# Performance work log

Hardware: AMD Instinct MI355X
Metric: run time of the kernel (lower is better)

## Reference

```python
import jax, jax.numpy as jnp
import numpy as np

B, T, H = 32, 2048, 1024

def setup_inputs() -> dict:
    key = jax.random.key(0)
    k1, k2, k3 = jax.random.split(key, 3)
    gru_output = jax.random.normal(k1, (B, T, H), dtype=jnp.float32)
    # Xavier uniform bounds
    lim_w = float(np.sqrt(6.0 / (H + H)))
    lim_c = float(np.sqrt(6.0 / (H + 1)))
    attention_weights = jax.random.uniform(k2, (H, H), minval=-lim_w, maxval=lim_w, dtype=jnp.float32)
    context_vector = jax.random.uniform(k3, (H, 1), minval=-lim_c, maxval=lim_c, dtype=jnp.float32)
    return {"gru_output": gru_output, "attention_weights": attention_weights, "context_vector": context_vector}

def reference(gru_output, attention_weights, context_vector):
    # score: [B, T, H]
    score = jnp.tanh(jnp.einsum('bth,hk->btk', gru_output, attention_weights))
    # logits: [B, T]
    logits = jnp.einsum('bth,h->bt', score, context_vector[:, 0])
    attn = jax.nn.softmax(logits, axis=1)  # over time dim
    # context: [B, H]
    context = jnp.einsum('bth,bt->bh', gru_output, attn)
    return (context, attn)
```

## Files before the change

kernel.cpp:

```cpp
#include <hip/hip_runtime.h>
#include <hip/hip_bf16.h>
#include <stdint.h>

#define B_DIM 32
#define T_DIM 2048
#define H_DIM 1024
#define M_DIM (B_DIM * T_DIM)
#define K_DIM H_DIM
#define N_DIM H_DIM
#define BK 32

typedef __attribute__((ext_vector_type(4))) float f32x4;
typedef __attribute__((ext_vector_type(8))) short short8;

__device__ __forceinline__ unsigned short f2bf(float x) {
  unsigned u = __float_as_uint(x);
  unsigned r = (u + 0x7FFFu + ((u >> 16) & 1u)) >> 16;
  return (unsigned short)r;
}

__device__ __forceinline__ float fast_tanh(float x) {
  x = fminf(fmaxf(x, -15.f), 15.f);
  float e = __expf(2.f * x);
  return (e - 1.f) / (e + 1.f);
}

__global__ void convert_g_kernel(const float* __restrict__ in,
                                 unsigned short* __restrict__ out) {
  size_t base = ((size_t)blockIdx.x * 256 + threadIdx.x) * 8;
  const float4* p = (const float4*)(in + base);
  float4 u0 = p[0];
  float4 u1 = p[1];
  short8 s;
  s[0] = (short)f2bf(u0.x); s[1] = (short)f2bf(u0.y);
  s[2] = (short)f2bf(u0.z); s[3] = (short)f2bf(u0.w);
  s[4] = (short)f2bf(u1.x); s[5] = (short)f2bf(u1.y);
  s[6] = (short)f2bf(u1.z); s[7] = (short)f2bf(u1.w);
  *(short8*)(out + base) = s;
}

__global__ void convert_w_kernel(const float* __restrict__ w,
                                 unsigned short* __restrict__ wt) {
  int g = blockIdx.x * 256 + threadIdx.x;
  int n = g >> 10;
  int k = g & 1023;
  wt[g] = f2bf(w[k * 1024 + n]);
}

__global__ __launch_bounds__(256) void gemm_tanh_logits(
    const unsigned short* __restrict__ A,
    const unsigned short* __restrict__ Bt,
    const float* __restrict__ cvec,
    float* __restrict__ logits) {
  __shared__ unsigned short sA[2][128 * BK];
  __shared__ unsigned short sB[2][128 * BK];

  const int tid = threadIdx.x;
  const int wid = tid >> 6;
  const int lane = tid & 63;

  int p = blockIdx.x;
  int logical = (p & 7) * 512 + (p >> 3);
  int mrow = logical >> 3;
  int ncol = logical & 7;

  const unsigned short* Abase = A + (size_t)mrow * 128 * K_DIM;
  const unsigned short* Bbase = Bt + (size_t)ncol * 128 * K_DIM;

  auto stage = [&](int buf, int kt) {
    const int r0 = wid * 32;
#pragma unroll
    for (int q = 0; q < 2; ++q) {
      int row = r0 + q * 16 + (lane >> 2);
      int gcol = kt * BK + (lane & 3) * 8;
      const unsigned short* ga = Abase + (size_t)row * K_DIM + gcol;
      const unsigned short* gb = Bbase + (size_t)row * K_DIM + gcol;
      unsigned short* la = &sA[buf][(r0 + q * 16) * BK];
      unsigned short* lb = &sB[buf][(r0 + q * 16) * BK];
      __builtin_amdgcn_global_load_lds(
          (const __attribute__((address_space(1))) unsigned int*)ga,
          (__attribute__((address_space(3))) unsigned int*)la, 16, 0, 0);
      __builtin_amdgcn_global_load_lds(
          (const __attribute__((address_space(1))) unsigned int*)gb,
          (__attribute__((address_space(3))) unsigned int*)lb, 16, 0, 0);
    }
  };

  f32x4 acc[4][4];
#pragma unroll
  for (int m = 0; m < 4; ++m)
#pragma unroll
    for (int n = 0; n < 4; ++n)
      acc[m][n] = (f32x4){0.f, 0.f, 0.f, 0.f};

  stage(0, 0);
  asm volatile("s_waitcnt vmcnt(0)" ::: "memory");
  __syncthreads();

  const int wr = (wid >> 1) * 64;
  const int wc = (wid & 1) * 64;
  const int frow = lane & 15;
  const int fk = (lane >> 4) * 8;

  int cur = 0;
  for (int kt = 0; kt < K_DIM / BK; ++kt) {
    if (kt + 1 < K_DIM / BK) stage(cur ^ 1, kt + 1);
    short8 a[4], b[4];
#pragma unroll
    for (int m = 0; m < 4; ++m)
      a[m] = *(const short8*)&sA[cur][(wr + m * 16 + frow) * BK + fk];
#pragma unroll
    for (int n = 0; n < 4; ++n)
      b[n] = *(const short8*)&sB[cur][(wc + n * 16 + frow) * BK + fk];
#pragma unroll
    for (int m = 0; m < 4; ++m)
#pragma unroll
      for (int n = 0; n < 4; ++n)
        acc[m][n] = __builtin_amdgcn_mfma_f32_16x16x32_bf16(a[m], b[n],
                                                            acc[m][n], 0, 0, 0);
    asm volatile("s_waitcnt vmcnt(0)" ::: "memory");
    __syncthreads();
    cur ^= 1;
  }

  const int cgrp = lane >> 4;
  const int cidx = lane & 15;
  const int colb = ncol * 128 + wc;
  const int rowb = mrow * 128 + wr;
#pragma unroll
  for (int m = 0; m < 4; ++m) {
    float s0 = 0.f, s1 = 0.f, s2 = 0.f, s3 = 0.f;
#pragma unroll
    for (int n = 0; n < 4; ++n) {
      float cw = cvec[colb + n * 16 + cidx];
      s0 += fast_tanh(acc[m][n][0]) * cw;
      s1 += fast_tanh(acc[m][n][1]) * cw;
      s2 += fast_tanh(acc[m][n][2]) * cw;
      s3 += fast_tanh(acc[m][n][3]) * cw;
    }
#pragma unroll
    for (int mask = 1; mask < 16; mask <<= 1) {
      s0 += __shfl_xor(s0, mask);
      s1 += __shfl_xor(s1, mask);
      s2 += __shfl_xor(s2, mask);
      s3 += __shfl_xor(s3, mask);
    }
    if (cidx == 0) {
      int row = rowb + m * 16 + cgrp * 4;
      atomicAdd(&logits[row + 0], s0);
      atomicAdd(&logits[row + 1], s1);
      atomicAdd(&logits[row + 2], s2);
      atomicAdd(&logits[row + 3], s3);
    }
  }
}

__global__ void softmax_kernel(float* __restrict__ la) {
  int b = blockIdx.x;
  float* row = la + (size_t)b * T_DIM;
  int tid = threadIdx.x;
  int wid = tid >> 6, lane = tid & 63;
  __shared__ float red[4];

  float v[8];
  float mx = -3.4e38f;
#pragma unroll
  for (int i = 0; i < 8; ++i) {
    v[i] = row[tid + i * 256];
    mx = fmaxf(mx, v[i]);
  }
#pragma unroll
  for (int mask = 32; mask >= 1; mask >>= 1) mx = fmaxf(mx, __shfl_xor(mx, mask));
  if (lane == 0) red[wid] = mx;
  __syncthreads();
  mx = fmaxf(fmaxf(red[0], red[1]), fmaxf(red[2], red[3]));
  __syncthreads();

  float sum = 0.f;
#pragma unroll
  for (int i = 0; i < 8; ++i) {
    v[i] = __expf(v[i] - mx);
    sum += v[i];
  }
#pragma unroll
  for (int mask = 32; mask >= 1; mask >>= 1) sum += __shfl_xor(sum, mask);
  if (lane == 0) red[wid] = sum;
  __syncthreads();
  sum = red[0] + red[1] + red[2] + red[3];
  float inv = 1.f / sum;
#pragma unroll
  for (int i = 0; i < 8; ++i) row[tid + i * 256] = v[i] * inv;
}

__global__ void context_kernel(const float* __restrict__ G,
                               const float* __restrict__ attn,
                               float* __restrict__ ctx) {
  int hc = blockIdx.x;
  int tc = blockIdx.y;
  int b = blockIdx.z;
  int h = hc * 256 + threadIdx.x;
  const float* g = G + (size_t)b * T_DIM * H_DIM + (size_t)tc * 256 * H_DIM + h;
  const float* a = attn + (size_t)b * T_DIM + tc * 256;
  float acc = 0.f;
#pragma unroll 4
  for (int t = 0; t < 256; ++t) acc += a[t] * g[(size_t)t * H_DIM];
  atomicAdd(&ctx[b * H_DIM + h], acc);
}

extern "C" void kernel_launch(void* const* d_in, const int* in_sizes, int n_in,
                              void* d_out, int out_size, void* d_ws, size_t ws_size,
                              hipStream_t stream) {
  const float* G = (const float*)d_in[0];
  const float* W = (const float*)d_in[1];
  const float* c = (const float*)d_in[2];
  float* out = (float*)d_out;
  float* ctx = out;
  float* attn = out + B_DIM * H_DIM;

  unsigned short* Gb = (unsigned short*)d_ws;
  unsigned short* Wt = (unsigned short*)((char*)d_ws +
                                         (size_t)M_DIM * K_DIM * 2);

  hipMemsetAsync(d_out, 0, (size_t)out_size * sizeof(float), stream);

  convert_g_kernel<<<M_DIM * K_DIM / (256 * 8), 256, 0, stream>>>(G, Gb);
  convert_w_kernel<<<N_DIM * K_DIM / 256, 256, 0, stream>>>(W, Wt);
  gemm_tanh_logits<<<(M_DIM / 128) * (N_DIM / 128), 256, 0, stream>>>(Gb, Wt, c, attn);
  softmax_kernel<<<B_DIM, 256, 0, stream>>>(attn);
  context_kernel<<<dim3(4, 8, 32), 256, 0, stream>>>(G, attn, ctx);
}
```

Measured before the change: 665.7 us.

## Retile GEMM to 256x256 with deep swizzled LDS pipeline; bf16 context pass

```diff
diff --git a/kernel.cpp b/kernel.cpp
--- a/kernel.cpp
+++ b/kernel.cpp
@@ -8,127 +8,175 @@
 #define M_DIM (B_DIM * T_DIM)
 #define K_DIM H_DIM
 #define N_DIM H_DIM
-#define BK 32
+
+#define BM 256
+#define BN 256
+#define BKT 32
+#define NTILES (K_DIM / BKT)
+#define DEPTH 3
 
 typedef __attribute__((ext_vector_type(4))) float f32x4;
 typedef __attribute__((ext_vector_type(8))) short short8;
+typedef __attribute__((ext_vector_type(4))) short short4v;
 
 __device__ __forceinline__ unsigned short f2bf(float x) {
   unsigned u = __float_as_uint(x);
-  unsigned r = (u + 0x7FFFu + ((u >> 16) & 1u)) >> 16;
-  return (unsigned short)r;
-}
-
+  return (unsigned short)((u + 0x7FFFu + ((u >> 16) & 1u)) >> 16);
+}
+__device__ __forceinline__ float bf2f(unsigned short h) {
+  return __uint_as_float(((unsigned)h) << 16);
+}
 __device__ __forceinline__ float fast_tanh(float x) {
-  x = fminf(fmaxf(x, -15.f), 15.f);
   float e = __expf(2.f * x);
-  return (e - 1.f) / (e + 1.f);
+  return 1.f - 2.f / (e + 1.f);
+}
+__device__ __forceinline__ int swz(int r, int s) {
+  return ((r >> 1) << 7) + (((((r & 1) << 2) | s) ^ ((r >> 1) & 7)) << 4);
 }
 
 __global__ void convert_g_kernel(const float* __restrict__ in,
                                  unsigned short* __restrict__ out) {
-  size_t base = ((size_t)blockIdx.x * 256 + threadIdx.x) * 8;
-  const float4* p = (const float4*)(in + base);
-  float4 u0 = p[0];
-  float4 u1 = p[1];
-  short8 s;
-  s[0] = (short)f2bf(u0.x); s[1] = (short)f2bf(u0.y);
-  s[2] = (short)f2bf(u0.z); s[3] = (short)f2bf(u0.w);
-  s[4] = (short)f2bf(u1.x); s[5] = (short)f2bf(u1.y);
-  s[6] = (short)f2bf(u1.z); s[7] = (short)f2bf(u1.w);
-  *(short8*)(out + base) = s;
+  size_t nvec = (size_t)M_DIM * K_DIM / 8;
+  size_t stride = (size_t)gridDim.x * blockDim.x;
+  for (size_t i = (size_t)blockIdx.x * blockDim.x + threadIdx.x; i < nvec;
+       i += stride) {
+    const float4* p = (const float4*)(in + i * 8);
+    float4 u0 = p[0], u1 = p[1];
+    short8 s;
+    s[0] = (short)f2bf(u0.x); s[1] = (short)f2bf(u0.y);
+    s[2] = (short)f2bf(u0.z); s[3] = (short)f2bf(u0.w);
+    s[4] = (short)f2bf(u1.x); s[5] = (short)f2bf(u1.y);
+    s[6] = (short)f2bf(u1.z); s[7] = (short)f2bf(u1.w);
+    *(short8*)(out + i * 8) = s;
+  }
 }
 
 __global__ void convert_w_kernel(const float* __restrict__ w,
                                  unsigned short* __restrict__ wt) {
-  int g = blockIdx.x * 256 + threadIdx.x;
-  int n = g >> 10;
-  int k = g & 1023;
-  wt[g] = f2bf(w[k * 1024 + n]);
-}
-
-__global__ __launch_bounds__(256) void gemm_tanh_logits(
+  __shared__ float tile[64][65];
+  int n0 = blockIdx.x * 64;
+  int k0 = blockIdx.y * 64;
+  int j = threadIdx.x & 63;
+  int i0 = threadIdx.x >> 6;
+#pragma unroll
+  for (int ii = 0; ii < 16; ++ii) {
+    int i = i0 * 16 + ii;
+    tile[i][j] = w[(size_t)(k0 + i) * H_DIM + n0 + j];
+  }
+  __syncthreads();
+#pragma unroll
+  for (int ii = 0; ii < 16; ++ii) {
+    int i = i0 * 16 + ii;
+    wt[(size_t)(n0 + i) * H_DIM + k0 + j] = f2bf(tile[j][i]);
+  }
+}
+
+__global__ __launch_bounds__(512, 2) void gemm_tanh_logits(
     const unsigned short* __restrict__ A,
     const unsigned short* __restrict__ Bt,
     const float* __restrict__ cvec,
     float* __restrict__ logits) {
-  __shared__ unsigned short sA[2][128 * BK];
-  __shared__ unsigned short sB[2][128 * BK];
+  __shared__ unsigned short lds[4][BM * BKT + BN * BKT];
 
   const int tid = threadIdx.x;
   const int wid = tid >> 6;
   const int lane = tid & 63;
 
   int p = blockIdx.x;
-  int logical = (p & 7) * 512 + (p >> 3);
-  int mrow = logical >> 3;
-  int ncol = logical & 7;
-
-  const unsigned short* Abase = A + (size_t)mrow * 128 * K_DIM;
-  const unsigned short* Bbase = Bt + (size_t)ncol * 128 * K_DIM;
-
-  auto stage = [&](int buf, int kt) {
-    const int r0 = wid * 32;
-#pragma unroll
-    for (int q = 0; q < 2; ++q) {
-      int row = r0 + q * 16 + (lane >> 2);
-      int gcol = kt * BK + (lane & 3) * 8;
-      const unsigned short* ga = Abase + (size_t)row * K_DIM + gcol;
-      const unsigned short* gb = Bbase + (size_t)row * K_DIM + gcol;
-      unsigned short* la = &sA[buf][(r0 + q * 16) * BK];
-      unsigned short* lb = &sB[buf][(r0 + q * 16) * BK];
+  int logical = (p & 7) * 128 + (p >> 3);
+  int mrow = logical >> 2;
+  int ncol = logical & 3;
+
+  const unsigned short* Ap = A + (size_t)mrow * BM * K_DIM;
+  const unsigned short* Bp = Bt + (size_t)ncol * BN * K_DIM;
+
+  auto stage_half = [&](int t, int h) {
+    int buf = t & 3;
+    const unsigned short* gp = h ? Bp : Ap;
+    unsigned short* base = &lds[buf][h ? BM * BKT : 0];
+#pragma unroll
+    for (int j = 0; j < 2; ++j) {
+      int o = j * 8192 + tid * 16;
+      int pr = o >> 7;
+      int v = ((o >> 4) & 7) ^ (pr & 7);
+      int r = (pr << 1) | (v >> 2);
+      int s = v & 3;
+      const unsigned short* ga = gp + (size_t)r * K_DIM + t * BKT + s * 8;
+      unsigned short* la = base + ((j * 8192 + wid * 1024) >> 1);
       __builtin_amdgcn_global_load_lds(
           (const __attribute__((address_space(1))) unsigned int*)ga,
           (__attribute__((address_space(3))) unsigned int*)la, 16, 0, 0);
-      __builtin_amdgcn_global_load_lds(
-          (const __attribute__((address_space(1))) unsigned int*)gb,
-          (__attribute__((address_space(3))) unsigned int*)lb, 16, 0, 0);
     }
   };
 
-  f32x4 acc[4][4];
-#pragma unroll
-  for (int m = 0; m < 4; ++m)
-#pragma unroll
-    for (int n = 0; n < 4; ++n)
-      acc[m][n] = (f32x4){0.f, 0.f, 0.f, 0.f};
-
-  stage(0, 0);
-  asm volatile("s_waitcnt vmcnt(0)" ::: "memory");
-  __syncthreads();
-
-  const int wr = (wid >> 1) * 64;
-  const int wc = (wid & 1) * 64;
-  const int frow = lane & 15;
-  const int fk = (lane >> 4) * 8;
-
-  int cur = 0;
-  for (int kt = 0; kt < K_DIM / BK; ++kt) {
-    if (kt + 1 < K_DIM / BK) stage(cur ^ 1, kt + 1);
+  const int wm = wid >> 2;
+  const int wn = wid & 3;
+  const int fr = lane & 15;
+  const int sl = lane >> 4;
+
+  const int aoff = swz(wm * 128 + fr, sl) >> 1;
+  const int boff = (swz(wn * 64 + fr, sl) >> 1) + BM * BKT;
+
+  f32x4 acc[8][4];
+#pragma unroll
+  for (int m = 0; m < 8; ++m)
+#pragma unroll
+    for (int n = 0; n < 4; ++n) acc[m][n] = (f32x4){0.f, 0.f, 0.f, 0.f};
+
+  stage_half(0, 0); stage_half(0, 1);
+  stage_half(1, 0); stage_half(1, 1);
+  stage_half(2, 0); stage_half(2, 1);
+  asm volatile("s_waitcnt vmcnt(8)" ::: "memory");
+  __builtin_amdgcn_s_barrier();
+
+  for (int t = 0; t < NTILES; ++t) {
+    const unsigned short* L0 = &lds[t & 3][0];
     short8 a[4], b[4];
-#pragma unroll
-    for (int m = 0; m < 4; ++m)
-      a[m] = *(const short8*)&sA[cur][(wr + m * 16 + frow) * BK + fk];
-#pragma unroll
-    for (int n = 0; n < 4; ++n)
-      b[n] = *(const short8*)&sB[cur][(wc + n * 16 + frow) * BK + fk];
+    asm volatile("" ::: "memory");
+    if (t + DEPTH < NTILES) stage_half(t + DEPTH, 0);
+#pragma unroll
+    for (int m = 0; m < 4; ++m) a[m] = *(const short8*)(L0 + aoff + m * 512);
+#pragma unroll
+    for (int n = 0; n < 4; ++n) b[n] = *(const short8*)(L0 + boff + n * 512);
+    __builtin_amdgcn_s_setprio(1);
 #pragma unroll
     for (int m = 0; m < 4; ++m)
 #pragma unroll
       for (int n = 0; n < 4; ++n)
         acc[m][n] = __builtin_amdgcn_mfma_f32_16x16x32_bf16(a[m], b[n],
                                                             acc[m][n], 0, 0, 0);
-    asm volatile("s_waitcnt vmcnt(0)" ::: "memory");
-    __syncthreads();
-    cur ^= 1;
+    __builtin_amdgcn_s_setprio(0);
+    asm volatile("" ::: "memory");
+    __builtin_amdgcn_s_barrier();
+    asm volatile("" ::: "memory");
+    if (t + DEPTH < NTILES) stage_half(t + DEPTH, 1);
+#pragma unroll
+    for (int m = 0; m < 4; ++m)
+      a[m] = *(const short8*)(L0 + aoff + (m + 4) * 512);
+    __builtin_amdgcn_s_setprio(1);
+#pragma unroll
+    for (int m = 0; m < 4; ++m)
+#pragma unroll
+      for (int n = 0; n < 4; ++n)
+        acc[m + 4][n] = __builtin_amdgcn_mfma_f32_16x16x32_bf16(
+            a[m], b[n], acc[m + 4][n], 0, 0, 0);
+    __builtin_amdgcn_s_setprio(0);
+    asm volatile("" ::: "memory");
+    if (t < NTILES - DEPTH)
+      asm volatile("s_waitcnt vmcnt(8)" ::: "memory");
+    else if (t == NTILES - DEPTH)
+      asm volatile("s_waitcnt vmcnt(4)" ::: "memory");
+    else if (t == NTILES - 2)
+      asm volatile("s_waitcnt vmcnt(0)" ::: "memory");
+    __builtin_amdgcn_s_barrier();
   }
 
   const int cgrp = lane >> 4;
   const int cidx = lane & 15;
-  const int colb = ncol * 128 + wc;
-  const int rowb = mrow * 128 + wr;
-#pragma unroll
-  for (int m = 0; m < 4; ++m) {
+  const int colb = ncol * BN + wn * 64;
+  const int rowb = mrow * BM + wm * 128;
+#pragma unroll
+  for (int m = 0; m < 8; ++m) {
     float s0 = 0.f, s1 = 0.f, s2 = 0.f, s3 = 0.f;
 #pragma unroll
     for (int n = 0; n < 4; ++n) {
@@ -192,19 +240,29 @@
   for (int i = 0; i < 8; ++i) row[tid + i * 256] = v[i] * inv;
 }
 
-__global__ void context_kernel(const float* __restrict__ G,
+__global__ void context_kernel(const unsigned short* __restrict__ Gb,
                                const float* __restrict__ attn,
                                float* __restrict__ ctx) {
-  int hc = blockIdx.x;
-  int tc = blockIdx.y;
-  int b = blockIdx.z;
-  int h = hc * 256 + threadIdx.x;
-  const float* g = G + (size_t)b * T_DIM * H_DIM + (size_t)tc * 256 * H_DIM + h;
-  const float* a = attn + (size_t)b * T_DIM + tc * 256;
-  float acc = 0.f;
+  int tc = blockIdx.x;
+  int b = blockIdx.y;
+  int h = threadIdx.x * 4;
+  const unsigned short* g = Gb + ((size_t)b * T_DIM + tc * 128) * H_DIM + h;
+  const float* a = attn + b * T_DIM + tc * 128;
+  float s0 = 0.f, s1 = 0.f, s2 = 0.f, s3 = 0.f;
 #pragma unroll 4
-  for (int t = 0; t < 256; ++t) acc += a[t] * g[(size_t)t * H_DIM];
-  atomicAdd(&ctx[b * H_DIM + h], acc);
+  for (int t = 0; t < 128; ++t) {
+    short4v v = *(const short4v*)(g + (size_t)t * H_DIM);
+    float w = a[t];
+    s0 += w * bf2f((unsigned short)v[0]);
+    s1 += w * bf2f((unsigned short)v[1]);
+    s2 += w * bf2f((unsigned short)v[2]);
+    s3 += w * bf2f((unsigned short)v[3]);
+  }
+  float* cb = ctx + b * H_DIM + h;
+  atomicAdd(cb + 0, s0);
+  atomicAdd(cb + 1, s1);
+  atomicAdd(cb + 2, s2);
+  atomicAdd(cb + 3, s3);
 }
 
 extern "C" void kernel_launch(void* const* d_in, const int* in_sizes, int n_in,
@@ -223,9 +281,9 @@
 
   hipMemsetAsync(d_out, 0, (size_t)out_size * sizeof(float), stream);
 
-  convert_g_kernel<<<M_DIM * K_DIM / (256 * 8), 256, 0, stream>>>(G, Gb);
-  convert_w_kernel<<<N_DIM * K_DIM / 256, 256, 0, stream>>>(W, Wt);
-  gemm_tanh_logits<<<(M_DIM / 128) * (N_DIM / 128), 256, 0, stream>>>(Gb, Wt, c, attn);
+  convert_g_kernel<<<4096, 256, 0, stream>>>(G, Gb);
+  convert_w_kernel<<<dim3(16, 16), 256, 0, stream>>>(W, Wt);
+  gemm_tanh_logits<<<1024, 512, 0, stream>>>(Gb, Wt, c, attn);
   softmax_kernel<<<B_DIM, 256, 0, stream>>>(attn);
-  context_kernel<<<dim3(4, 8, 32), 256, 0, stream>>>(G, attn, ctx);
-}
+  context_kernel<<<dim3(16, 32), 256, 0, stream>>>(Gb, attn, ctx);
+}
```

Measured after the change: 571.6 us. 14.1% less time.
